# Kernel optimization log

Measured on AMD Instinct MI355X. Metric: run time of the kernel, lower is better.

Reference implementation:

```python
import jax, jax.numpy as jnp
import numpy as np

B, NPG = 128, 512            # graphs, nodes per graph (batch is contiguous & uniform)
N = B * NPG                  # 65536 nodes
DEG = 8
E = N * DEG                  # 524288 edges
F_IN, NHID = 128, 64
H, C = 3, NHID               # GAT heads, out channels per head
HC = H * C                   # 192
NCLS = 10
RATIO = 0.5
NEG_SLOPE = 0.2


def setup_inputs() -> dict:
    key = jax.random.key(0)
    ks = jax.random.split(key, 24)
    x = jax.random.normal(ks[0], (N, F_IN), jnp.float32)
    # edges constrained within each graph (graphs are contiguous blocks of NPG nodes)
    offs = jnp.repeat(jnp.arange(B, dtype=jnp.int32) * NPG, NPG * DEG)
    src = jax.random.randint(ks[1], (E,), 0, NPG, dtype=jnp.int32) + offs
    dst = jax.random.randint(ks[2], (E,), 0, NPG, dtype=jnp.int32) + offs
    edge_index = jnp.stack([src, dst], axis=0)
    edge_attr = jax.random.normal(ks[3], (E, 2), jnp.float32)
    batch = jnp.repeat(jnp.arange(B, dtype=jnp.int32), NPG)

    def lin(k, o, i):
        return jax.random.normal(k, (o, i), jnp.float32) / np.float32(np.sqrt(i))

    return {
        "x": x, "edge_index": edge_index, "edge_attr": edge_attr, "batch": batch,
        # lin: num_features -> nhid//2
        "W_lin": lin(ks[4], NHID // 2, F_IN), "b_lin": jnp.zeros((NHID // 2,), jnp.float32),
        # GATConv(nhid//2 -> nhid, heads=3, edge_dim=2)
        "W_src": lin(ks[5], HC, NHID // 2),
        "att_src": jax.random.normal(ks[6], (H, C), jnp.float32) / np.float32(np.sqrt(C)),
        "att_dst": jax.random.normal(ks[7], (H, C), jnp.float32) / np.float32(np.sqrt(C)),
        "W_edge": lin(ks[8], HC, 2),
        "att_edge": jax.random.normal(ks[9], (H, C), jnp.float32) / np.float32(np.sqrt(C)),
        "b_gat": jnp.zeros((HC,), jnp.float32),
        # SAGPool score layer: GCNConv(nhid*3 -> 1)
        "W_gcn": lin(ks[10], 1, HC), "b_gcn": jnp.zeros((1,), jnp.float32),
        # classifier MLP
        "W1": lin(ks[11], NHID, 2 * HC), "b1": jnp.zeros((NHID,), jnp.float32),
        "W2": lin(ks[12], NHID // 2, NHID), "b2": jnp.zeros((NHID // 2,), jnp.float32),
        "W3": lin(ks[13], NCLS, NHID // 2), "b3": jnp.zeros((NCLS,), jnp.float32),
    }


def reference(x, edge_index, edge_attr, batch,
              W_lin, b_lin, W_src, att_src, att_dst, W_edge, att_edge, b_gat,
              W_gcn, b_gcn, W1, b1, W2, b2, W3, b3):
    src, dst = edge_index[0], edge_index[1]

    # ---- lin + ELU -------------------------------------------------------
    h = jax.nn.elu(x @ W_lin.T + b_lin)                       # [N, nhid//2]

    # ---- GATConv(heads=3, edge_dim=2), add_self_loops fill_value='mean' --
    loop = jnp.arange(N, dtype=src.dtype)
    cnt = jax.ops.segment_sum(jnp.ones((E,), h.dtype), dst, num_segments=N)
    loop_attr = jax.ops.segment_sum(edge_attr, dst, num_segments=N) / jnp.maximum(cnt, 1.0)[:, None]
    s_full = jnp.concatenate([src, loop])
    d_full = jnp.concatenate([dst, loop])
    ea_full = jnp.concatenate([edge_attr, loop_attr], axis=0)  # [E+N, 2]

    xp = (h @ W_src.T).reshape(N, H, C)                        # projected per-head feats
    a_src = (xp * att_src).sum(-1)                             # [N, H]
    a_dst = (xp * att_dst).sum(-1)                             # [N, H]
    ef = (ea_full @ W_edge.T).reshape(-1, H, C)
    a_edge = (ef * att_edge).sum(-1)                           # [E+N, H]

    alpha = jax.nn.leaky_relu(a_src[s_full] + a_dst[d_full] + a_edge, NEG_SLOPE)
    m = jax.ops.segment_max(alpha, d_full, num_segments=N)     # scatter-softmax over dst
    ealpha = jnp.exp(alpha - m[d_full])
    denom = jax.ops.segment_sum(ealpha, d_full, num_segments=N)
    alpha = ealpha / (denom[d_full] + 1e-16)                   # [E+N, H]

    out = jax.ops.segment_sum(alpha[:, :, None] * xp[s_full], d_full, num_segments=N)
    x1 = jax.nn.relu(out.reshape(N, HC) + b_gat)               # [N, 192]

    # ---- SAGPool: GCNConv score + per-graph top-k (mask form) ------------
    xw = x1 @ W_gcn.T                                          # [N, 1]
    deg = jax.ops.segment_sum(jnp.ones((E,), x1.dtype), dst, num_segments=N) + 1.0
    dinv = jax.lax.rsqrt(deg)
    agg = jax.ops.segment_sum((dinv[src] * dinv[dst])[:, None] * xw[src], dst, num_segments=N)
    score = (agg + (dinv ** 2)[:, None] * xw + b_gcn)[:, 0]    # [N]

    k = int(np.ceil(RATIO * NPG))                              # nodes kept per graph
    s2 = score.reshape(B, NPG)
    rank = jnp.argsort(jnp.argsort(-s2, axis=1), axis=1)
    mask = rank < k                                            # [B, NPG] top-k selection

    xs = (x1 * jnp.tanh(score)[:, None]).reshape(B, NPG, HC)
    gmp = jnp.max(jnp.where(mask[:, :, None], xs, -jnp.inf), axis=1)   # [B, 192]
    gap = jnp.sum(jnp.where(mask[:, :, None], xs, 0.0), axis=1) / k    # [B, 192]
    r = jnp.concatenate([gmp, gap], axis=1)                    # [B, 384]

    # ---- classifier MLP (dropout is identity in eval) ---------------------
    r = jax.nn.relu(r @ W1.T + b1)
    r = jax.nn.relu(r @ W2.T + b2)
    return jax.nn.log_softmax(r @ W3.T + b3, axis=-1)          # [B, num_classes]
```

## Files before the change

kernel.cpp:

```cpp
#include <hip/hip_runtime.h>
#include <hip/hip_bf16.h>
#include <math.h>

#define NN   65536
#define EE   524288
#define BB   128
#define NPGC 512
#define HCC  192
#define KSEL 256
#define NEG  0.2f
#define PSEG 16
#define SEGN (NPGC / PSEG)
#define MAXD 40
#define SLOTS ((size_t)NN * MAXD)
#define EPG   4096
#define HSTR  36

__global__ __launch_bounds__(192) void k_v(
    const float* __restrict__ W_src, const float* __restrict__ att_src,
    const float* __restrict__ att_dst, const float* __restrict__ W_edge,
    const float* __restrict__ att_edge, float* __restrict__ vbuf) {
    __shared__ float red[6];
    int t = threadIdx.x;
    if (t < 6) red[t] = 0.f;
    __syncthreads();
    {
        float ae = att_edge[t];
        int h = t >> 6;
        atomicAdd(&red[h],     W_edge[2 * t]     * ae);
        atomicAdd(&red[3 + h], W_edge[2 * t + 1] * ae);
    }
    if (t < 96) {
        int h = t >> 5, k = t & 31;
        float vs = 0.f, vd = 0.f;
        for (int c = 0; c < 64; ++c) {
            float w = W_src[(h * 64 + c) * 32 + k];
            vs += w * att_src[h * 64 + c];
            vd += w * att_dst[h * 64 + c];
        }
        vbuf[t] = vs;
        vbuf[96 + t] = vd;
    }
    __syncthreads();
    if (t < 6) vbuf[192 + t] = red[t];
}

__global__ __launch_bounds__(128) void k_feat(
    const float* __restrict__ x, const float* __restrict__ W_lin,
    const float* __restrict__ b_lin, const float* __restrict__ W_src,
    const float* __restrict__ vbuf,
    float* __restrict__ xp, float* __restrict__ ap_s, float* __restrict__ ap_d) {
    __shared__ float Wl[128 * HSTR];
    __shared__ float hs[128 * HSTR];
    __shared__ float apl[128][6];
    int t = threadIdx.x;
    for (int i = t; i < 4096; i += 128) {
        int j = i >> 7, k = i & 127;
        Wl[k * HSTR + j] = W_lin[i];
    }
    int bx = blockIdx.x;
    int xcd = bx & 7, j2 = bx >> 3;
    int g = xcd + 8 * (j2 >> 2);
    int nb = g * NPGC + (j2 & 3) * 128;
    int sl = t >> 5;
    int nl0 = t & 31;
    int j0 = (sl & 3) * 8;
    float vS[24], vD[24];
#pragma unroll
    for (int h = 0; h < 3; ++h)
#pragma unroll
        for (int c = 0; c < 8; ++c) {
            vS[h * 8 + c] = vbuf[h * 32 + j0 + c];
            vD[h * 8 + c] = vbuf[96 + h * 32 + j0 + c];
        }
    float acc[4][8];
#pragma unroll
    for (int r = 0; r < 4; ++r)
#pragma unroll
        for (int c = 0; c < 8; ++c) acc[r][c] = b_lin[j0 + c];
    const float4* xr0 = (const float4*)(x + (size_t)(nb + nl0) * 128);
    const float4* xr1 = (const float4*)(x + (size_t)(nb + nl0 + 32) * 128);
    const float4* xr2 = (const float4*)(x + (size_t)(nb + nl0 + 64) * 128);
    const float4* xr3 = (const float4*)(x + (size_t)(nb + nl0 + 96) * 128);
    __syncthreads();
#pragma unroll 2
    for (int q = 0; q < 32; ++q) {
        float4 xa = xr0[q], xb = xr1[q], xc = xr2[q], xd = xr3[q];
        float fa[4] = {xa.x, xa.y, xa.z, xa.w};
        float fb[4] = {xb.x, xb.y, xb.z, xb.w};
        float fc[4] = {xc.x, xc.y, xc.z, xc.w};
        float fd[4] = {xd.x, xd.y, xd.z, xd.w};
#pragma unroll
        for (int kk = 0; kk < 4; ++kk) {
            const float4* w4 = (const float4*)&Wl[(q * 4 + kk) * HSTR + j0];
            float4 wA = w4[0], wB = w4[1];
            float w8[8] = {wA.x, wA.y, wA.z, wA.w, wB.x, wB.y, wB.z, wB.w};
#pragma unroll
            for (int c = 0; c < 8; ++c) {
                acc[0][c] += fa[kk] * w8[c];
                acc[1][c] += fb[kk] * w8[c];
                acc[2][c] += fc[kk] * w8[c];
                acc[3][c] += fd[kk] * w8[c];
            }
        }
    }
    float ps[4][3], pd[4][3];
#pragma unroll
    for (int r = 0; r < 4; ++r) {
#pragma unroll
        for (int h = 0; h < 3; ++h) { ps[r][h] = 0.f; pd[r][h] = 0.f; }
#pragma unroll
        for (int c = 0; c < 8; ++c) {
            float v = acc[r][c];
            v = v > 0.f ? v : expm1f(v);
            acc[r][c] = v;
#pragma unroll
            for (int h = 0; h < 3; ++h) {
                ps[r][h] += v * vS[h * 8 + c];
                pd[r][h] += v * vD[h * 8 + c];
            }
        }
        float4* hw = (float4*)&hs[(nl0 + 32 * r) * HSTR + j0];
        hw[0] = make_float4(acc[r][0], acc[r][1], acc[r][2], acc[r][3]);
        hw[1] = make_float4(acc[r][4], acc[r][5], acc[r][6], acc[r][7]);
    }
#pragma unroll
    for (int r = 0; r < 4; ++r)
#pragma unroll
        for (int h = 0; h < 3; ++h) {
            ps[r][h] += __shfl_xor(ps[r][h], 32, 64);
            pd[r][h] += __shfl_xor(pd[r][h], 32, 64);
        }
    if (t < 32) {
#pragma unroll
        for (int r = 0; r < 4; ++r)
#pragma unroll
            for (int h = 0; h < 3; ++h) {
                apl[nl0 + 32 * r][h] = ps[r][h];
                apl[nl0 + 32 * r][3 + h] = pd[r][h];
            }
    }
    __syncthreads();
    if (t >= 64 && t < 96) {
#pragma unroll
        for (int r = 0; r < 4; ++r) {
            int n = nb + nl0 + 32 * r;
#pragma unroll
            for (int h = 0; h < 3; ++h) {
                ap_s[(size_t)h * NN + n] = apl[nl0 + 32 * r][h] + ps[r][h];
                ap_d[(size_t)h * NN + n] = apl[nl0 + 32 * r][3 + h] + pd[r][h];
            }
        }
    }
    int lane = t & 63, wave = t >> 6;
    float wreg[96];
#pragma unroll
    for (int h = 0; h < 3; ++h) {
        const float4* wp = (const float4*)(W_src + (h * 64 + lane) * 32);
#pragma unroll
        for (int q = 0; q < 8; ++q) {
            float4 w = wp[q];
            wreg[h * 32 + 4 * q]     = w.x;
            wreg[h * 32 + 4 * q + 1] = w.y;
            wreg[h * 32 + 4 * q + 2] = w.z;
            wreg[h * 32 + 4 * q + 3] = w.w;
        }
    }
    int n0 = wave * 64;
    for (int nd = 0; nd < 64; ++nd) {
        int nl2 = n0 + nd;
        const float4* hr = (const float4*)&hs[nl2 * HSTR];
        float a0 = 0.f, a1 = 0.f, a2 = 0.f;
#pragma unroll
        for (int q = 0; q < 8; ++q) {
            float4 hv = hr[q];
            a0 += hv.x*wreg[4*q] + hv.y*wreg[4*q+1] + hv.z*wreg[4*q+2] + hv.w*wreg[4*q+3];
            a1 += hv.x*wreg[32+4*q] + hv.y*wreg[32+4*q+1] + hv.z*wreg[32+4*q+2] + hv.w*wreg[32+4*q+3];
            a2 += hv.x*wreg[64+4*q] + hv.y*wreg[64+4*q+1] + hv.z*wreg[64+4*q+2] + hv.w*wreg[64+4*q+3];
        }
        size_t nbase = (size_t)(nb + nl2) * HCC;
        xp[nbase + lane] = a0;
        xp[nbase + 64 + lane] = a1;
        xp[nbase + 128 + lane] = a2;
    }
}

__global__ __launch_bounds__(1024) void k_edges(
    const int* __restrict__ ei, const float* __restrict__ ea,
    const float* __restrict__ ap_s, const float* __restrict__ ap_d,
    const float* __restrict__ vbuf,
    int* __restrict__ fill, float4* __restrict__ slotA) {
    __shared__ int   s_pos[NPGC];
    __shared__ float s_la[NPGC * 2];
    __shared__ float s_as[NPGC * 3], s_ad[NPGC * 3];
    int b = blockIdx.x, t = threadIdx.x;
    int g = (b & 7) + 8 * (b >> 3);
    int nbase = g * NPGC;
    int ebase = g * EPG;
    if (t < NPGC) s_pos[t] = 0;
    s_la[t] = 0.f;
    for (int i = t; i < NPGC * 3; i += 1024) {
        int h = i >> 9, nl = i & (NPGC - 1);
        s_as[nl * 3 + h] = ap_s[(size_t)h * NN + nbase + nl];
        s_ad[nl * 3 + h] = ap_d[(size_t)h * NN + nbase + nl];
    }
    float ac[6];
#pragma unroll
    for (int h = 0; h < 6; ++h) ac[h] = vbuf[192 + h];
    int4  se  = ((const int4*)(ei + ebase))[t];
    int4  de  = ((const int4*)(ei + EE + ebase))[t];
    float4 a0 = ((const float4*)(ea + 2 * ebase))[2 * t];
    float4 a1 = ((const float4*)(ea + 2 * ebase))[2 * t + 1];
    __syncthreads();

    int   ss[4] = {se.x, se.y, se.z, se.w};
    int   dd[4] = {de.x, de.y, de.z, de.w};
    float e0v[4] = {a0.x, a0.z, a1.x, a1.z};
    float e1v[4] = {a0.y, a0.w, a1.y, a1.w};
#pragma unroll
    for (int k = 0; k < 4; ++k) {
        int s = ss[k], d = dd[k];
        int sl = s & (NPGC - 1), dl = d & (NPGC - 1);
        float e0 = e0v[k], e1 = e1v[k];
        atomicAdd(&s_la[2 * dl],     e0);
        atomicAdd(&s_la[2 * dl + 1], e1);
        float v[3];
#pragma unroll
        for (int h = 0; h < 3; ++h) {
            float a = s_as[sl * 3 + h] + s_ad[dl * 3 + h] +
                      e0 * ac[h] + e1 * ac[3 + h];
            v[h] = a >= 0.f ? a : NEG * a;
        }
        int pos = atomicAdd(&s_pos[dl], 1);
        if (pos < MAXD - 1)
            slotA[(size_t)(nbase + dl) * MAXD + 1 + pos] =
                make_float4(v[0], v[1], v[2], __int_as_float(s));
    }
    __syncthreads();
    if (t < NPGC) {
        int cnt = s_pos[t];
        int n = nbase + t;
        fill[n] = cnt;
        float inv = 1.f / fmaxf((float)cnt, 1.f);
        float l0 = s_la[2 * t] * inv, l1 = s_la[2 * t + 1] * inv;
        float v[3];
#pragma unroll
        for (int h = 0; h < 3; ++h) {
            float a = s_as[t * 3 + h] + s_ad[t * 3 + h] +
                      l0 * ac[h] + l1 * ac[3 + h];
            v[h] = a >= 0.f ? a : NEG * a;
        }
        slotA[(size_t)n * MAXD] = make_float4(v[0], v[1], v[2],
                                              __int_as_float(n));
    }
}

__global__ __launch_bounds__(256) void k_agg(
    const int* __restrict__ fill, const float4* __restrict__ slotA,
    const float* __restrict__ xp,
    const float* __restrict__ b_gat, const float* __restrict__ W_gcn,
    float* __restrict__ x1, float* __restrict__ xwd, float* __restrict__ dinv) {
    __shared__ float2 wsl[4][3][65];
    int wave = threadIdx.x >> 6, lane = threadIdx.x & 63;
    int b = blockIdx.x;
    int xcd = b & 7, j = b >> 3;
    int g = (j >> 7) * 8 + xcd;
    int n = g * NPGC + (j & 127) * 4 + wave;

    int ctrue = fill[n];
    int cnt = ctrue < (MAXD - 1) ? ctrue : (MAXD - 1);
    int tot = cnt + 1;

    if (lane < tot) {
        float4 pk = slotA[(size_t)n * MAXD + lane];
        wsl[wave][0][lane] = make_float2(__expf(pk.x), pk.w);
        wsl[wave][1][lane] = make_float2(__expf(pk.y), pk.w);
        wsl[wave][2][lane] = make_float2(__expf(pk.z), pk.w);
    }
    bool act = lane < 48;
    int head = act ? (lane >> 4) : 0;
    const float2* wp = &wsl[wave][head][0];
    const float4* xp4 = (const float4*)xp;
    float ax = 0.f, ay = 0.f, az = 0.f, aw = 0.f, den = 0.f;
    int s = 0;
    for (; s + 3 < tot; s += 4) {
        float2 wsA = wp[s],     wsB = wp[s + 1];
        float2 wsC = wp[s + 2], wsD = wp[s + 3];
        den += (wsA.x + wsB.x) + (wsC.x + wsD.x);
        if (act) {
            float4 vA = xp4[(size_t)__float_as_int(wsA.y) * 48 + lane];
            float4 vB = xp4[(size_t)__float_as_int(wsB.y) * 48 + lane];
            float4 vC = xp4[(size_t)__float_as_int(wsC.y) * 48 + lane];
            float4 vD = xp4[(size_t)__float_as_int(wsD.y) * 48 + lane];
            ax += wsA.x * vA.x + wsB.x * vB.x + wsC.x * vC.x + wsD.x * vD.x;
            ay += wsA.x * vA.y + wsB.x * vB.y + wsC.x * vC.y + wsD.x * vD.y;
            az += wsA.x * vA.z + wsB.x * vB.z + wsC.x * vC.z + wsD.x * vD.z;
            aw += wsA.x * vA.w + wsB.x * vB.w + wsC.x * vC.w + wsD.x * vD.w;
        }
    }
    for (; s < tot; ++s) {
        float2 wsA = wp[s];
        den += wsA.x;
        if (act) {
            float4 vA = xp4[(size_t)__float_as_int(wsA.y) * 48 + lane];
            ax += wsA.x * vA.x; ay += wsA.x * vA.y;
            az += wsA.x * vA.z; aw += wsA.x * vA.w;
        }
    }
    float p = 0.f;
    if (act) {
        float id = 1.f / (den + 1e-16f);
        float4 bg = ((const float4*)b_gat)[lane];
        float4 v;
        v.x = fmaxf(ax * id + bg.x, 0.f);
        v.y = fmaxf(ay * id + bg.y, 0.f);
        v.z = fmaxf(az * id + bg.z, 0.f);
        v.w = fmaxf(aw * id + bg.w, 0.f);
        ((float4*)x1)[(size_t)n * 48 + lane] = v;
        float4 wg = ((const float4*)W_gcn)[lane];
        p = v.x * wg.x + v.y * wg.y + v.z * wg.z + v.w * wg.w;
    }
#pragma unroll
    for (int msk = 32; msk > 0; msk >>= 1) p += __shfl_xor(p, msk, 64);
    if (lane == 0) {
        float dv = rsqrtf((float)ctrue + 1.f);
        xwd[n] = p * dv;
        dinv[n] = dv;
    }
}

__global__ __launch_bounds__(256) void k_score(
    const int* __restrict__ fill, const float4* __restrict__ slotA,
    const float* __restrict__ xwd, const float* __restrict__ dinv,
    const float* __restrict__ b_gcn, float* __restrict__ score) {
    int wave = threadIdx.x >> 6, lane = threadIdx.x & 63;
    int b = blockIdx.x;
    int xcd = b & 7, j = b >> 3;
    int g = (j >> 7) * 8 + xcd;
    int n = g * NPGC + (j & 127) * 4 + wave;

    int ctrue = fill[n];
    int cnt = ctrue < (MAXD - 1) ? ctrue : (MAXD - 1);
    float acc = 0.f;
    if (lane <= cnt) {
        int src = __float_as_int(
            ((const float*)slotA)[((size_t)n * MAXD + lane) * 4 + 3]);
        acc = xwd[src];
    }
#pragma unroll
    for (int msk = 32; msk > 0; msk >>= 1) acc += __shfl_xor(acc, msk, 64);
    if (lane == 0) score[n] = b_gcn[0] + dinv[n] * acc;
}

__global__ __launch_bounds__(192) void k_poolrank(
    const float* __restrict__ score, const float* __restrict__ x1,
    float* __restrict__ pmax, float* __restrict__ psum) {
    __shared__ float sc[NPGC];
    __shared__ float ts_s[SEGN];
    __shared__ int sel_s[SEGN];
    int b = blockIdx.x;
    int xcd = b & 7, gslot = (b >> 3) & 15, seg = b >> 7;
    int g = gslot * 8 + xcd;
    int t = threadIdx.x;
    int gbase = g * NPGC;
    for (int i = t; i < NPGC; i += 192) sc[i] = score[gbase + i];
    __syncthreads();
    if (t < SEGN) {
        int iloc = seg * SEGN + t;
        float si = sc[iloc];
        int rank = 0;
        for (int j = 0; j < NPGC; ++j) {
            float sj = sc[j];
            rank += (sj > si) || (sj == si && j < iloc);
        }
        sel_s[t] = (rank < KSEL) ? 1 : 0;
        ts_s[t] = tanhf(si);
    }
    __syncthreads();
    int nb = gbase + seg * SEGN;
    float mx = -1e30f, sm = 0.f;
    for (int i = 0; i < SEGN; ++i) {
        if (sel_s[i]) {
            float v = x1[(size_t)(nb + i) * HCC + t] * ts_s[i];
            mx = fmaxf(mx, v);
            sm += v;
        }
    }
    size_t pb = (size_t)(g * PSEG + seg) * HCC + t;
    pmax[pb] = mx;
    psum[pb] = sm;
}

__global__ __launch_bounds__(384) void k_mlp(
    const float* __restrict__ pmax, const float* __restrict__ psum,
    const float* __restrict__ W1, const float* __restrict__ b1,
    const float* __restrict__ W2, const float* __restrict__ b2,
    const float* __restrict__ W3, const float* __restrict__ b3,
    float* __restrict__ out) {
    __shared__ float rs[384], part[384], h1[64], h2[32], lg[10], mls;
    int g = blockIdx.x, t = threadIdx.x;
    if (t < HCC) {
        float mx = -1e30f, sm = 0.f;
#pragma unroll
        for (int s = 0; s < PSEG; ++s) {
            mx = fmaxf(mx, pmax[(size_t)(g * PSEG + s) * HCC + t]);
            sm += psum[(size_t)(g * PSEG + s) * HCC + t];
        }
        rs[t] = mx;
        rs[HCC + t] = sm * (1.f / (float)KSEL);
    }
    __syncthreads();
    {
        int o = t / 6, sl = t - o * 6;
        const float* wr = W1 + o * 384 + sl * 64;
        const float* rr = rs + sl * 64;
        float s = 0.f;
#pragma unroll 8
        for (int k = 0; k < 64; ++k) s += rr[k] * wr[k];
        part[t] = s;
    }
    __syncthreads();
    if (t < 64) {
        float s = b1[t];
#pragma unroll
        for (int j = 0; j < 6; ++j) s += part[t * 6 + j];
        h1[t] = fmaxf(s, 0.f);
    }
    __syncthreads();
    if (t < 256) {
        int o = t >> 3, sl = t & 7;
        const float* wr = W2 + o * 64 + sl * 8;
        const float* hr = h1 + sl * 8;
        float s = 0.f;
#pragma unroll
        for (int k = 0; k < 8; ++k) s += hr[k] * wr[k];
        part[t] = s;
    }
    __syncthreads();
    if (t < 32) {
        float s = b2[t];
#pragma unroll
        for (int j = 0; j < 8; ++j) s += part[t * 8 + j];
        h2[t] = fmaxf(s, 0.f);
    }
    __syncthreads();
    if (t < 10) {
        float s = b3[t];
        for (int k = 0; k < 32; ++k) s += h2[k] * W3[t * 32 + k];
        lg[t] = s;
    }
    __syncthreads();
    if (t == 0) {
        float mx = lg[0];
        for (int j = 1; j < 10; ++j) mx = fmaxf(mx, lg[j]);
        float se = 0.f;
        for (int j = 0; j < 10; ++j) se += expf(lg[j] - mx);
        mls = mx + logf(se);
    }
    __syncthreads();
    if (t < 10) out[g * 10 + t] = lg[t] - mls;
}

extern "C" void kernel_launch(void* const* d_in, const int* in_sizes, int n_in,
                              void* d_out, int out_size, void* d_ws, size_t ws_size,
                              hipStream_t stream) {
    const float* x        = (const float*)d_in[0];
    const int*   ei       = (const int*)d_in[1];
    const float* ea       = (const float*)d_in[2];
    const float* W_lin    = (const float*)d_in[4];
    const float* b_lin    = (const float*)d_in[5];
    const float* W_src    = (const float*)d_in[6];
    const float* att_src  = (const float*)d_in[7];
    const float* att_dst  = (const float*)d_in[8];
    const float* W_edge   = (const float*)d_in[9];
    const float* att_edge = (const float*)d_in[10];
    const float* b_gat    = (const float*)d_in[11];
    const float* W_gcn    = (const float*)d_in[12];
    const float* b_gcn    = (const float*)d_in[13];
    const float* W1 = (const float*)d_in[14]; const float* b1 = (const float*)d_in[15];
    const float* W2 = (const float*)d_in[16]; const float* b2 = (const float*)d_in[17];
    const float* W3 = (const float*)d_in[18]; const float* b3 = (const float*)d_in[19];
    float* out = (float*)d_out;

    char* ws = (char*)d_ws;
    size_t off = 0;
    auto alloc = [&](size_t bytes) {
        size_t r = off;
        off += (bytes + 255) & ~(size_t)255;
        return r;
    };
    float* xp      = (float*)(ws + alloc((size_t)NN * HCC * 4));
    float* x1      = (float*)(ws + alloc((size_t)NN * HCC * 4));
    int*   fill    = (int*)(ws + alloc((size_t)NN * 4));
    float* ap_s    = (float*)(ws + alloc((size_t)NN * 3 * 4));
    float* ap_d    = (float*)(ws + alloc((size_t)NN * 3 * 4));
    float4* slotA  = (float4*)(ws + alloc(SLOTS * 16));
    float* xwd     = (float*)(ws + alloc((size_t)NN * 4));
    float* dinv    = (float*)(ws + alloc((size_t)NN * 4));
    float* score   = (float*)(ws + alloc((size_t)NN * 4));
    float* vbuf    = (float*)(ws + alloc(256 * 4));
    float* pmax    = (float*)(ws + alloc((size_t)BB * PSEG * HCC * 4));
    float* psum    = (float*)(ws + alloc((size_t)BB * PSEG * HCC * 4));

    k_v<<<1, 192, 0, stream>>>(W_src, att_src, att_dst, W_edge, att_edge, vbuf);
    k_feat<<<512, 128, 0, stream>>>(x, W_lin, b_lin, W_src, vbuf,
                                    xp, ap_s, ap_d);
    k_edges<<<BB, 1024, 0, stream>>>(ei, ea, ap_s, ap_d, vbuf, fill, slotA);
    k_agg<<<NN / 4, 256, 0, stream>>>(fill, slotA, xp, b_gat, W_gcn,
                                      x1, xwd, dinv);
    k_score<<<NN / 4, 256, 0, stream>>>(fill, slotA, xwd, dinv, b_gcn, score);
    k_poolrank<<<BB * PSEG, 192, 0, stream>>>(score, x1, pmax, psum);
    k_mlp<<<BB, 384, 0, stream>>>(pmax, psum, W1, b1, W2, b2, W3, b3, out);
}
```

Measured before the change: 259.5 us.

## Fold attention-vector precompute into k_feat and k_edges, drop k_v launch

Result: no change. 262.9 us (+1.3%).

```diff
diff --git a/kernel.cpp b/kernel.cpp
--- a/kernel.cpp
+++ b/kernel.cpp
@@ -16,19 +16,25 @@
 #define EPG   4096
 #define HSTR  36
 
-__global__ __launch_bounds__(192) void k_v(
-    const float* __restrict__ W_src, const float* __restrict__ att_src,
-    const float* __restrict__ att_dst, const float* __restrict__ W_edge,
-    const float* __restrict__ att_edge, float* __restrict__ vbuf) {
-    __shared__ float red[6];
+__device__ __forceinline__ int nodeblock_base(int bx) {
+    int xcd = bx & 7, j = bx >> 3;
+    int g = xcd + 8 * (j >> 1);
+    return g * NPGC + (j & 1) * 256;
+}
+
+__global__ __launch_bounds__(256) void k_feat(
+    const float* __restrict__ x, const float* __restrict__ W_lin,
+    const float* __restrict__ b_lin, const float* __restrict__ W_src,
+    const float* __restrict__ att_src, const float* __restrict__ att_dst,
+    float* __restrict__ xp, float* __restrict__ ap_s, float* __restrict__ ap_d) {
+    __shared__ float Wl[128 * HSTR];
+    __shared__ float hs[256 * HSTR];
+    __shared__ float vsd[192];
+    __shared__ float apf[256][6];
     int t = threadIdx.x;
-    if (t < 6) red[t] = 0.f;
-    __syncthreads();
-    {
-        float ae = att_edge[t];
-        int h = t >> 6;
-        atomicAdd(&red[h],     W_edge[2 * t]     * ae);
-        atomicAdd(&red[3 + h], W_edge[2 * t + 1] * ae);
+    for (int i = t; i < 4096; i += 256) {
+        int j = i >> 7, k = i & 127;
+        Wl[k * HSTR + j] = W_lin[i];
     }
     if (t < 96) {
         int h = t >> 5, k = t & 31;
@@ -38,50 +44,23 @@
             vs += w * att_src[h * 64 + c];
             vd += w * att_dst[h * 64 + c];
         }
-        vbuf[t] = vs;
-        vbuf[96 + t] = vd;
-    }
-    __syncthreads();
-    if (t < 6) vbuf[192 + t] = red[t];
-}
-
-__global__ __launch_bounds__(128) void k_feat(
-    const float* __restrict__ x, const float* __restrict__ W_lin,
-    const float* __restrict__ b_lin, const float* __restrict__ W_src,
-    const float* __restrict__ vbuf,
-    float* __restrict__ xp, float* __restrict__ ap_s, float* __restrict__ ap_d) {
-    __shared__ float Wl[128 * HSTR];
-    __shared__ float hs[128 * HSTR];
-    __shared__ float apl[128][6];
-    int t = threadIdx.x;
-    for (int i = t; i < 4096; i += 128) {
-        int j = i >> 7, k = i & 127;
-        Wl[k * HSTR + j] = W_lin[i];
-    }
-    int bx = blockIdx.x;
-    int xcd = bx & 7, j2 = bx >> 3;
-    int g = xcd + 8 * (j2 >> 2);
-    int nb = g * NPGC + (j2 & 3) * 128;
-    int sl = t >> 5;
-    int nl0 = t & 31;
-    int j0 = (sl & 3) * 8;
-    float vS[24], vD[24];
-#pragma unroll
-    for (int h = 0; h < 3; ++h)
-#pragma unroll
-        for (int c = 0; c < 8; ++c) {
-            vS[h * 8 + c] = vbuf[h * 32 + j0 + c];
-            vD[h * 8 + c] = vbuf[96 + h * 32 + j0 + c];
-        }
+        vsd[t] = vs;
+        vsd[96 + t] = vd;
+    }
+    for (int i = t; i < 1536; i += 256) ((float*)apf)[i] = 0.f;
+    int nb = nodeblock_base(blockIdx.x);
+    int sl = t >> 6;
+    int nl0 = t & 63;
+    int j0 = sl * 8;
     float acc[4][8];
 #pragma unroll
     for (int r = 0; r < 4; ++r)
 #pragma unroll
         for (int c = 0; c < 8; ++c) acc[r][c] = b_lin[j0 + c];
     const float4* xr0 = (const float4*)(x + (size_t)(nb + nl0) * 128);
-    const float4* xr1 = (const float4*)(x + (size_t)(nb + nl0 + 32) * 128);
-    const float4* xr2 = (const float4*)(x + (size_t)(nb + nl0 + 64) * 128);
-    const float4* xr3 = (const float4*)(x + (size_t)(nb + nl0 + 96) * 128);
+    const float4* xr1 = (const float4*)(x + (size_t)(nb + nl0 + 64) * 128);
+    const float4* xr2 = (const float4*)(x + (size_t)(nb + nl0 + 128) * 128);
+    const float4* xr3 = (const float4*)(x + (size_t)(nb + nl0 + 192) * 128);
     __syncthreads();
 #pragma unroll 2
     for (int q = 0; q < 32; ++q) {
@@ -104,11 +83,9 @@
             }
         }
     }
-    float ps[4][3], pd[4][3];
 #pragma unroll
     for (int r = 0; r < 4; ++r) {
-#pragma unroll
-        for (int h = 0; h < 3; ++h) { ps[r][h] = 0.f; pd[r][h] = 0.f; }
+        float ps[3] = {0.f, 0.f, 0.f}, pd[3] = {0.f, 0.f, 0.f};
 #pragma unroll
         for (int c = 0; c < 8; ++c) {
             float v = acc[r][c];
@@ -116,40 +93,27 @@
             acc[r][c] = v;
 #pragma unroll
             for (int h = 0; h < 3; ++h) {
-                ps[r][h] += v * vS[h * 8 + c];
-                pd[r][h] += v * vD[h * 8 + c];
+                ps[h] += v * vsd[h * 32 + j0 + c];
+                pd[h] += v * vsd[96 + h * 32 + j0 + c];
             }
         }
-        float4* hw = (float4*)&hs[(nl0 + 32 * r) * HSTR + j0];
+        int nl = nl0 + 64 * r;
+        float4* hw = (float4*)&hs[nl * HSTR + j0];
         hw[0] = make_float4(acc[r][0], acc[r][1], acc[r][2], acc[r][3]);
         hw[1] = make_float4(acc[r][4], acc[r][5], acc[r][6], acc[r][7]);
-    }
-#pragma unroll
-    for (int r = 0; r < 4; ++r)
 #pragma unroll
         for (int h = 0; h < 3; ++h) {
-            ps[r][h] += __shfl_xor(ps[r][h], 32, 64);
-            pd[r][h] += __shfl_xor(pd[r][h], 32, 64);
-        }
-    if (t < 32) {
-#pragma unroll
-        for (int r = 0; r < 4; ++r)
-#pragma unroll
-            for (int h = 0; h < 3; ++h) {
-                apl[nl0 + 32 * r][h] = ps[r][h];
-                apl[nl0 + 32 * r][3 + h] = pd[r][h];
-            }
-    }
-    __syncthreads();
-    if (t >= 64 && t < 96) {
-#pragma unroll
-        for (int r = 0; r < 4; ++r) {
-            int n = nb + nl0 + 32 * r;
-#pragma unroll
-            for (int h = 0; h < 3; ++h) {
-                ap_s[(size_t)h * NN + n] = apl[nl0 + 32 * r][h] + ps[r][h];
-                ap_d[(size_t)h * NN + n] = apl[nl0 + 32 * r][3 + h] + pd[r][h];
-            }
+            atomicAdd(&apf[nl][h], ps[h]);
+            atomicAdd(&apf[nl][3 + h], pd[h]);
+        }
+    }
+    __syncthreads();
+    {
+        int n = nb + t;
+#pragma unroll
+        for (int h = 0; h < 3; ++h) {
+            ap_s[(size_t)h * NN + n] = apf[t][h];
+            ap_d[(size_t)h * NN + n] = apf[t][3 + h];
         }
     }
     int lane = t & 63, wave = t >> 6;
@@ -188,30 +152,38 @@
 __global__ __launch_bounds__(1024) void k_edges(
     const int* __restrict__ ei, const float* __restrict__ ea,
     const float* __restrict__ ap_s, const float* __restrict__ ap_d,
-    const float* __restrict__ vbuf,
+    const float* __restrict__ W_edge, const float* __restrict__ att_edge,
     int* __restrict__ fill, float4* __restrict__ slotA) {
     __shared__ int   s_pos[NPGC];
     __shared__ float s_la[NPGC * 2];
     __shared__ float s_as[NPGC * 3], s_ad[NPGC * 3];
+    __shared__ float s_ac[6];
     int b = blockIdx.x, t = threadIdx.x;
     int g = (b & 7) + 8 * (b >> 3);
     int nbase = g * NPGC;
     int ebase = g * EPG;
     if (t < NPGC) s_pos[t] = 0;
     s_la[t] = 0.f;
+    if (t < 6) {
+        int h = t % 3, part = t / 3;
+        float s = 0.f;
+        for (int c = h * 64; c < h * 64 + 64; ++c)
+            s += W_edge[2 * c + part] * att_edge[c];
+        s_ac[part * 3 + h] = s;
+    }
     for (int i = t; i < NPGC * 3; i += 1024) {
         int h = i >> 9, nl = i & (NPGC - 1);
         s_as[nl * 3 + h] = ap_s[(size_t)h * NN + nbase + nl];
         s_ad[nl * 3 + h] = ap_d[(size_t)h * NN + nbase + nl];
     }
-    float ac[6];
-#pragma unroll
-    for (int h = 0; h < 6; ++h) ac[h] = vbuf[192 + h];
     int4  se  = ((const int4*)(ei + ebase))[t];
     int4  de  = ((const int4*)(ei + EE + ebase))[t];
     float4 a0 = ((const float4*)(ea + 2 * ebase))[2 * t];
     float4 a1 = ((const float4*)(ea + 2 * ebase))[2 * t + 1];
     __syncthreads();
+    float ac[6];
+#pragma unroll
+    for (int h = 0; h < 6; ++h) ac[h] = s_ac[h];
 
     int   ss[4] = {se.x, se.y, se.z, se.w};
     int   dd[4] = {de.x, de.y, de.z, de.w};
@@ -498,14 +470,13 @@
     float* xwd     = (float*)(ws + alloc((size_t)NN * 4));
     float* dinv    = (float*)(ws + alloc((size_t)NN * 4));
     float* score   = (float*)(ws + alloc((size_t)NN * 4));
-    float* vbuf    = (float*)(ws + alloc(256 * 4));
     float* pmax    = (float*)(ws + alloc((size_t)BB * PSEG * HCC * 4));
     float* psum    = (float*)(ws + alloc((size_t)BB * PSEG * HCC * 4));
 
-    k_v<<<1, 192, 0, stream>>>(W_src, att_src, att_dst, W_edge, att_edge, vbuf);
-    k_feat<<<512, 128, 0, stream>>>(x, W_lin, b_lin, W_src, vbuf,
+    k_feat<<<256, 256, 0, stream>>>(x, W_lin, b_lin, W_src, att_src, att_dst,
                                     xp, ap_s, ap_d);
-    k_edges<<<BB, 1024, 0, stream>>>(ei, ea, ap_s, ap_d, vbuf, fill, slotA);
+    k_edges<<<BB, 1024, 0, stream>>>(ei, ea, ap_s, ap_d, W_edge, att_edge,
+                                     fill, slotA);
     k_agg<<<NN / 4, 256, 0, stream>>>(fill, slotA, xp, b_gat, W_gcn,
                                       x1, xwd, dinv);
     k_score<<<NN / 4, 256, 0, stream>>>(fill, slotA, xwd, dinv, b_gcn, score);
```
